# Performance work log

Hardware: AMD Instinct MI355X
Metric: run time of the kernel (lower is better)

The kernel has to match this reference:

```python
import jax, jax.numpy as jnp
import numpy as np

D = 1024
H = 16
HD = D // H  # 64
FF = 4 * D
EPS = 1e-5

def _layernorm(x, g, b):
    mu = jnp.mean(x, axis=-1, keepdims=True)
    var = jnp.mean((x - mu) ** 2, axis=-1, keepdims=True)
    return (x - mu) * jax.lax.rsqrt(var + EPS) * g + b

def _apply_rotary(x, cos, sin):
    # x: [B,H,T,HD]; cos/sin: [T,HD//2] broadcast over B,H
    d = x.shape[-1] // 2
    x1, x2 = x[..., :d], x[..., d:]
    return jnp.concatenate([x1 * cos - x2 * sin, x2 * cos + x1 * sin], axis=-1)

def setup_inputs() -> dict:
    key = jax.random.key(0)
    ks = jax.random.split(key, 12)
    B, T = 4, 2048
    s = 0.02
    return {
        "x": jax.random.normal(ks[0], (B, T, D), jnp.float32),
        "rope_cos": jax.random.uniform(ks[1], (T, HD // 2), jnp.float32),
        "rope_sin": jax.random.uniform(ks[2], (T, HD // 2), jnp.float32),
        "ln1_g": jnp.ones((D,), jnp.float32),
        "ln1_b": jnp.zeros((D,), jnp.float32),
        "Wqkv": jax.random.normal(ks[3], (D, 3 * D), jnp.float32) * s,
        "bqkv": jnp.zeros((3 * D,), jnp.float32),
        "Wo": jax.random.normal(ks[4], (D, D), jnp.float32) * s,
        "bo": jnp.zeros((D,), jnp.float32),
        "ln2_g": jnp.ones((D,), jnp.float32),
        "ln2_b": jnp.zeros((D,), jnp.float32),
        "W1": jax.random.normal(ks[5], (D, FF), jnp.float32) * s,
        "b1": jnp.zeros((FF,), jnp.float32),
        "W2": jax.random.normal(ks[6], (FF, D), jnp.float32) * s,
        "b2": jnp.zeros((D,), jnp.float32),
    }

def reference(x, rope_cos, rope_sin, ln1_g, ln1_b, Wqkv, bqkv, Wo, bo, ln2_g, ln2_b, W1, b1, W2, b2):
    B, T, _ = x.shape
    h = _layernorm(x, ln1_g, ln1_b)
    qkv = (h @ Wqkv + bqkv).reshape(B, T, 3, H, HD)
    qkv = jnp.transpose(qkv, (2, 0, 3, 1, 4))  # [3,B,H,T,HD]
    q, k, v = qkv[0], qkv[1], qkv[2]
    q = _apply_rotary(q, rope_cos, rope_sin)
    k = _apply_rotary(k, rope_cos, rope_sin)
    scale = 1.0 / jnp.sqrt(jnp.float32(HD))
    scores = jnp.einsum('bhqd,bhkd->bhqk', q, k) * scale
    probs = jax.nn.softmax(scores, axis=-1)
    attn = jnp.einsum('bhqk,bhkd->bhqd', probs, v)
    attn = jnp.transpose(attn, (0, 2, 1, 3)).reshape(B, T, D)
    x = x + attn @ Wo + bo
    h2 = _layernorm(x, ln2_g, ln2_b)
    mlp = jax.nn.gelu(h2 @ W1 + b1, approximate=False) @ W2 + b2
    return x + mlp
```

## Files before the change

kernel.cpp:

```cpp
#include <hip/hip_runtime.h>
#include <hip/hip_bf16.h>
#include <math.h>

typedef __bf16 bf16x8 __attribute__((ext_vector_type(8)));
typedef float f32x4 __attribute__((ext_vector_type(4)));
typedef float f32x16 __attribute__((ext_vector_type(16)));
typedef unsigned short u16x8 __attribute__((ext_vector_type(8)));
typedef unsigned short u16x4 __attribute__((ext_vector_type(4)));
typedef unsigned int u32x4 __attribute__((ext_vector_type(4)));

#define DEV __device__ __forceinline__

DEV unsigned short f2bf(float f) { __bf16 h = (__bf16)f; return __builtin_bit_cast(unsigned short, h); }
DEV float bf2f(unsigned short u) { __bf16 h = __builtin_bit_cast(__bf16, u); return (float)h; }
DEV unsigned int pk2(float a, float b) {
  return (unsigned int)f2bf(a) | ((unsigned int)f2bf(b) << 16);
}

DEV void async_cp16(const void* g, void* l) {
  __builtin_amdgcn_global_load_lds((const __attribute__((address_space(1))) void*)g,
                                   (__attribute__((address_space(3))) void*)l, 16, 0, 0);
}


__global__ __launch_bounds__(256) void ln_kernel(const float* __restrict__ in,
    const float* __restrict__ g, const float* __restrict__ b,
    unsigned short* __restrict__ out)
{
  const int row = blockIdx.x;
  const int tid = threadIdx.x;
  const float4 v = ((const float4*)(in + (size_t)row * 1024))[tid];
  float s  = v.x + v.y + v.z + v.w;
  float sq = v.x*v.x + v.y*v.y + v.z*v.z + v.w*v.w;
  for (int m = 1; m < 64; m <<= 1) { s += __shfl_xor(s, m); sq += __shfl_xor(sq, m); }
  __shared__ float red[8];
  const int wave = tid >> 6;
  if ((tid & 63) == 0) { red[wave] = s; red[4 + wave] = sq; }
  __syncthreads();
  s  = red[0] + red[1] + red[2] + red[3];
  sq = red[4] + red[5] + red[6] + red[7];
  const float mu = s * (1.0f / 1024.0f);
  const float var = sq * (1.0f / 1024.0f) - mu * mu;
  const float rs = rsqrtf(var + 1e-5f);
  const float4 gv = ((const float4*)g)[tid];
  const float4 bv = ((const float4*)b)[tid];
  u16x4 o;
  o[0] = f2bf((v.x - mu) * rs * gv.x + bv.x);
  o[1] = f2bf((v.y - mu) * rs * gv.y + bv.y);
  o[2] = f2bf((v.z - mu) * rs * gv.z + bv.z);
  o[3] = f2bf((v.w - mu) * rs * gv.w + bv.w);
  *(u16x4*)(out + (size_t)row * 1024 + tid * 4) = o;
}

__global__ __launch_bounds__(256) void wtrans_kernel(const float* __restrict__ in,
    unsigned short* __restrict__ out, int K, int N)
{
  __shared__ float tile[32][33];
  const int n0 = blockIdx.x * 32, k0 = blockIdx.y * 32;
  const int r = threadIdx.x >> 5, c = threadIdx.x & 31;
  for (int p = 0; p < 4; ++p)
    tile[r + p * 8][c] = in[(size_t)(k0 + r + p * 8) * N + n0 + c];
  __syncthreads();
  for (int p = 0; p < 4; ++p)
    out[(size_t)(n0 + r + p * 8) * K + k0 + c] = f2bf(tile[c][r + p * 8]);
}

enum { EPI_QKV = 0, EPI_ATTNO = 1, EPI_GELU = 2, EPI_FINAL = 3 };

template <int EPI>
__global__ __launch_bounds__(256, 3) void gemm_bt(
    const unsigned short* __restrict__ A,
    const unsigned short* __restrict__ Bt,
    const float* __restrict__ bias,
    const float* __restrict__ resid,
    void* __restrict__ out,
    int M, int N, int K,
    const float* __restrict__ rc, const float* __restrict__ rsn,
    unsigned short* __restrict__ vout)
{
  __shared__ unsigned short lA[8192] __attribute__((aligned(16)));
  __shared__ unsigned short lB[8192] __attribute__((aligned(16)));
  const int tid = threadIdx.x;
  const int lane = tid & 63, wave = tid >> 6;
  const int l15 = lane & 15, quad = lane >> 4;
  const int bm = blockIdx.x * 128, bn = blockIdx.y * 128;
  const int wm = (wave & 1) * 64, wn = (wave >> 1) * 64;

  const unsigned short* ga[4]; const unsigned short* gb[4];
  unsigned short* la_dst[4]; unsigned short* lb_dst[4];
  for (int it = 0; it < 4; ++it) {
    const int s = it * 256 + tid;
    const int row = s >> 3;
    const int ch = (s & 7) ^ (row & 7);
    ga[it] = A  + (size_t)(bm + row) * K + ch * 8;
    gb[it] = Bt + (size_t)(bn + row) * K + ch * 8;
    const int base = (it * 256 + wave * 64) * 8;
    la_dst[it] = lA + base;
    lb_dst[it] = lB + base;
  }
  int offA[2][4], offB[2][4];
  for (int ks = 0; ks < 2; ++ks)
    for (int i = 0; i < 4; ++i) {
      int row = wm + i * 16 + l15;
      offA[ks][i] = (row * 8 + ((ks * 4 + quad) ^ (row & 7))) * 8;
      row = wn + i * 16 + l15;
      offB[ks][i] = (row * 8 + ((ks * 4 + quad) ^ (row & 7))) * 8;
    }

  f32x4 acc[4][4];
  for (int i = 0; i < 4; ++i)
    for (int j = 0; j < 4; ++j)
      acc[i][j] = f32x4{0.f, 0.f, 0.f, 0.f};

  for (int k0 = 0; k0 < K; k0 += 64) {
    for (int it = 0; it < 4; ++it) async_cp16(ga[it], la_dst[it]);
    for (int it = 0; it < 4; ++it) async_cp16(gb[it], lb_dst[it]);
    for (int it = 0; it < 4; ++it) { ga[it] += 64; gb[it] += 64; }
    __syncthreads();
    for (int ks = 0; ks < 2; ++ks) {
      bf16x8 af[4], bfr[4];
      for (int i = 0; i < 4; ++i) af[i]  = *(const bf16x8*)(lA + offA[ks][i]);
      for (int j = 0; j < 4; ++j) bfr[j] = *(const bf16x8*)(lB + offB[ks][j]);
      for (int i = 0; i < 4; ++i)
        for (int j = 0; j < 4; ++j)
          acc[i][j] = __builtin_amdgcn_mfma_f32_16x16x32_bf16(af[i], bfr[j], acc[i][j], 0, 0, 0);
    }
    __syncthreads();
  }

  float bvals[4];
  for (int j = 0; j < 4; ++j) bvals[j] = bias[bn + wn + j * 16 + l15];

  if constexpr (EPI == EPI_QKV) {
    const int cn = bn + wn;
    const int sec = cn >> 10;
    if (sec == 2) {
      const int b = bm >> 11;
      const int hh = (cn & 1023) >> 6;
      for (int i = 0; i < 4; ++i) {
        const int t0 = (bm + wm + i * 16 + quad * 4) & 2047;
        for (int j = 0; j < 4; ++j) {
          const int d = j * 16 + l15;
          u16x4 o;
          for (int r = 0; r < 4; ++r) o[r] = f2bf(acc[i][j][r] + bvals[j]);
          *(u16x4*)(vout + ((size_t)((b * 16 + hh) * 64 + d)) * 2048 + t0) = o;
        }
      }
    } else {
      const float qscale = (sec == 0) ? 0.18033688f : 1.0f;
      unsigned short* qkvout = (unsigned short*)out;
      for (int i = 0; i < 4; ++i) {
        for (int r = 0; r < 4; ++r) {
          const int row = bm + wm + i * 16 + quad * 4 + r;
          const int t = row & 2047;
          for (int j = 0; j < 2; ++j) {
            const int d = j * 16 + l15;
            const float v1 = acc[i][j][r] + bvals[j];
            const float v2 = acc[i][j + 2][r] + bvals[j + 2];
            const float c = rc[t * 32 + d], s = rsn[t * 32 + d];
            const float o1 = (v1 * c - v2 * s) * qscale;
            const float o2 = (v2 * c + v1 * s) * qscale;
            const size_t base = (size_t)row * 3072 + cn + d;
            qkvout[base] = f2bf(o1);
            qkvout[base + 32] = f2bf(o2);
          }
        }
      }
    }
  } else {
    for (int i = 0; i < 4; ++i) {
      for (int r = 0; r < 4; ++r) {
        const size_t row = bm + wm + i * 16 + quad * 4 + r;
        for (int j = 0; j < 4; ++j) {
          const size_t col = bn + wn + j * 16 + l15;
          const float v = acc[i][j][r] + bvals[j];
          const size_t idx = row * (size_t)N + col;
          if constexpr (EPI == EPI_ATTNO) {
            ((float*)out)[idx] = resid[idx] + v;
          } else if constexpr (EPI == EPI_GELU) {
            const float gl = 0.5f * v * (1.0f + erff(v * 0.70710678118f));
            ((unsigned short*)out)[idx] = f2bf(gl);
          } else {
            ((float*)out)[idx] = resid[idx] + v;
          }
        }
      }
    }
  }
}

__global__ __launch_bounds__(256, 4) void attn_kernel(
    const unsigned short* __restrict__ qkv,
    const unsigned short* __restrict__ vt,
    unsigned short* __restrict__ outb)
{
  __shared__ unsigned short Ks[2][4096] __attribute__((aligned(16)));
  __shared__ unsigned short Vs[2][4096] __attribute__((aligned(16)));
  __shared__ float Sred[128];

  const int tid = threadIdx.x;
  const int lane = tid & 63, wave = tid >> 6;
  const int l31 = lane & 31, hl = lane >> 5;
  const int bh = blockIdx.y, b = bh >> 4, h = bh & 15;
  const int q0 = blockIdx.x * 128;
  const int qsub = wave * 32;

  bf16x8 qf[4];
  {
    const unsigned short* qp = qkv + (size_t)(b * 2048 + q0 + qsub + l31) * 3072 + h * 64 + hl * 8;
    for (int kc = 0; kc < 4; ++kc) qf[kc] = *(const bf16x8*)(qp + kc * 16);
  }

  const int s0 = wave * 128 + lane, s1 = s0 + 64;
  const int r0 = s0 >> 3, c0 = (lane & 7) ^ (r0 & 7);
  const int r1 = s1 >> 3, c1 = (lane & 7) ^ (r1 & 7);
  const unsigned short* kbase = qkv + (size_t)(b * 2048) * 3072 + 1024 + h * 64;
  const unsigned short* ks0 = kbase + (size_t)r0 * 3072 + c0 * 8;
  const unsigned short* ks1 = kbase + (size_t)r1 * 3072 + c1 * 8;
  const unsigned short* vbase = vt + (size_t)bh * 64 * 2048;
  const unsigned short* vs0 = vbase + (size_t)r0 * 2048 + c0 * 8;
  const unsigned short* vs1 = vbase + (size_t)r1 * 2048 + c1 * 8;
  unsigned short* kd[2] = { Ks[0] + wave * 1024, Ks[1] + wave * 1024 };
  unsigned short* vd[2] = { Vs[0] + wave * 1024, Vs[1] + wave * 1024 };

  int offK[2][4], offV[2][4];
  for (int g = 0; g < 2; ++g)
    for (int kc = 0; kc < 4; ++kc) {
      const int rk = g * 32 + l31;
      offK[g][kc] = (rk * 8 + ((2 * kc + hl) ^ (rk & 7))) * 8;
    }
  for (int dn = 0; dn < 2; ++dn)
    for (int t = 0; t < 4; ++t) {
      const int rv = dn * 32 + l31;
      offV[dn][t] = (rv * 8 + ((2 * t + hl) ^ (rv & 7))) * 8;
    }

  f32x16 accO[2];
  for (int dn = 0; dn < 2; ++dn)
    for (int i = 0; i < 16; ++i) accO[dn][i] = 0.f;
  float rsum = 0.f;

  async_cp16(ks0, kd[0]);
  async_cp16(ks1, kd[0] + 512);
  async_cp16(vs0, vd[0]);
  async_cp16(vs1, vd[0] + 512);

  for (int kt = 0; kt < 32; ++kt) {
    const int cur = kt & 1, nxt = cur ^ 1;
    __syncthreads();
    if (kt < 31) {
      const size_t ko = (size_t)(kt + 1) * 64 * 3072;
      const int vo = (kt + 1) * 64;
      async_cp16(ks0 + ko, kd[nxt]);
      async_cp16(ks1 + ko, kd[nxt] + 512);
      async_cp16(vs0 + vo, vd[nxt]);
      async_cp16(vs1 + vo, vd[nxt] + 512);
    }
    for (int g = 0; g < 2; ++g) {
      f32x16 accS;
      for (int i = 0; i < 16; ++i) accS[i] = 0.f;
      __builtin_amdgcn_s_setprio(1);
      for (int kc = 0; kc < 4; ++kc) {
        const bf16x8 kf = *(const bf16x8*)(Ks[cur] + offK[g][kc]);
        accS = __builtin_amdgcn_mfma_f32_32x32x16_bf16(kf, qf[kc], accS, 0, 0, 0);
      }
      __builtin_amdgcn_s_setprio(0);
      float p[16];
      for (int i = 0; i < 16; ++i) {
        p[i] = __builtin_amdgcn_exp2f(accS[i]);
        rsum += p[i];
      }
      for (int c = 0; c < 2; ++c) {
        const unsigned int xlo0 = pk2(p[8 * c + 0], p[8 * c + 1]);
        const unsigned int xlo1 = pk2(p[8 * c + 2], p[8 * c + 3]);
        const unsigned int xhi0 = pk2(p[8 * c + 4], p[8 * c + 5]);
        const unsigned int xhi1 = pk2(p[8 * c + 6], p[8 * c + 7]);
        const auto sw0 = __builtin_amdgcn_permlane32_swap(xlo0, xhi0, false, false);
        const auto sw1 = __builtin_amdgcn_permlane32_swap(xlo1, xhi1, false, false);
        u32x4 w;
        w[0] = sw0[0];
        w[1] = sw1[0];
        w[2] = sw0[1];
        w[3] = sw1[1];
        const bf16x8 pf = __builtin_bit_cast(bf16x8, w);
        const int t = 2 * g + c;
        __builtin_amdgcn_s_setprio(1);
        for (int dn = 0; dn < 2; ++dn) {
          const bf16x8 vf = *(const bf16x8*)(Vs[cur] + offV[dn][t]);
          accO[dn] = __builtin_amdgcn_mfma_f32_32x32x16_bf16(pf, vf, accO[dn], 0, 0, 0);
        }
        __builtin_amdgcn_s_setprio(0);
      }
    }
  }

  {
    const float rs2 = rsum + __shfl_xor(rsum, 32);
    if (hl == 0) Sred[qsub + l31] = rs2;
  }
  __syncthreads();
  for (int reg = 0; reg < 16; ++reg) {
    const int rq = qsub + (reg & 3) + 8 * (reg >> 2) + 4 * hl;
    const float inv = 1.0f / Sred[rq];
    const size_t row = (size_t)(b * 2048 + q0 + rq);
    for (int dn = 0; dn < 2; ++dn)
      outb[row * 1024 + h * 64 + dn * 32 + l31] = f2bf(accO[dn][reg] * inv);
  }
}

extern "C" void kernel_launch(void* const* d_in, const int* in_sizes, int n_in,
                              void* d_out, int out_size, void* d_ws, size_t ws_size,
                              hipStream_t stream)
{
  const float* x        = (const float*)d_in[0];
  const float* rope_cos = (const float*)d_in[1];
  const float* rope_sin = (const float*)d_in[2];
  const float* ln1_g    = (const float*)d_in[3];
  const float* ln1_b    = (const float*)d_in[4];
  const float* Wqkv     = (const float*)d_in[5];
  const float* bqkv     = (const float*)d_in[6];
  const float* Wo       = (const float*)d_in[7];
  const float* bo       = (const float*)d_in[8];
  const float* ln2_g    = (const float*)d_in[9];
  const float* ln2_b    = (const float*)d_in[10];
  const float* W1       = (const float*)d_in[11];
  const float* b1       = (const float*)d_in[12];
  const float* W2       = (const float*)d_in[13];
  const float* b2       = (const float*)d_in[14];
  float* outp = (float*)d_out;

  char* ws = (char*)d_ws;
  size_t off = 0;
  auto alloc = [&](size_t bytes) -> void* {
    void* p = ws + off;
    off += (bytes + 255) & ~(size_t)255;
    return p;
  };
  unsigned short* h1    = (unsigned short*)alloc(8192ull * 1024 * 2);
  unsigned short* wqkvT = (unsigned short*)alloc(3072ull * 1024 * 2);
  unsigned short* woT   = (unsigned short*)alloc(1024ull * 1024 * 2);
  unsigned short* w1T   = (unsigned short*)alloc(4096ull * 1024 * 2);
  unsigned short* w2T   = (unsigned short*)alloc(1024ull * 4096 * 2);
  unsigned short* qkv   = (unsigned short*)alloc(8192ull * 3072 * 2);
  unsigned short* vtb   = (unsigned short*)alloc(64ull * 64 * 2048 * 2);
  unsigned short* h2    = (unsigned short*)alloc(8192ull * 1024 * 2);
  unsigned short* ffb   = (unsigned short*)alloc(8192ull * 4096 * 2);

  wtrans_kernel<<<dim3(96, 32), 256, 0, stream>>>(Wqkv, wqkvT, 1024, 3072);
  wtrans_kernel<<<dim3(32, 32), 256, 0, stream>>>(Wo, woT, 1024, 1024);
  wtrans_kernel<<<dim3(128, 32), 256, 0, stream>>>(W1, w1T, 1024, 4096);
  wtrans_kernel<<<dim3(32, 128), 256, 0, stream>>>(W2, w2T, 4096, 1024);

  ln_kernel<<<8192, 256, 0, stream>>>(x, ln1_g, ln1_b, h1);
  gemm_bt<EPI_QKV><<<dim3(64, 24), 256, 0, stream>>>(h1, wqkvT, bqkv, nullptr, qkv,
                                                     8192, 3072, 1024, rope_cos, rope_sin, vtb);
  attn_kernel<<<dim3(16, 64), 256, 0, stream>>>(qkv, vtb, h1);
  gemm_bt<EPI_ATTNO><<<dim3(64, 8), 256, 0, stream>>>(h1, woT, bo, x, d_out,
                                                      8192, 1024, 1024, nullptr, nullptr, nullptr);
  ln_kernel<<<8192, 256, 0, stream>>>(outp, ln2_g, ln2_b, h2);
  gemm_bt<EPI_GELU><<<dim3(64, 32), 256, 0, stream>>>(h2, w1T, b1, nullptr, ffb,
                                                      8192, 4096, 1024, nullptr, nullptr, nullptr);
  gemm_bt<EPI_FINAL><<<dim3(64, 8), 256, 0, stream>>>(ffb, w2T, b2, outp, d_out,
                                                      8192, 1024, 4096, nullptr, nullptr, nullptr);
}
```

Before: 495.8 us.

## Process two 32-row query groups per wave in attention to reuse K/V tiles

Each wave in the attention kernel now handles 64 query rows as two 32-row groups instead of one. Each K fragment and V fragment loaded from LDS feeds two MFMAs. The block covers 256 queries, so the grid is halved and K/V global/LDS traffic per query drops by half. In exchange register pressure roughly doubles (launch bounds lowered to 2 blocks/SM) and there are fewer blocks to fill the GPU (512 blocks).

```diff
diff --git a/kernel.cpp b/kernel.cpp
--- a/kernel.cpp
+++ b/kernel.cpp
@@ -189,26 +189,26 @@
   }
 }
 
-__global__ __launch_bounds__(256, 4) void attn_kernel(
+__global__ __launch_bounds__(256, 2) void attn_kernel(
     const unsigned short* __restrict__ qkv,
     const unsigned short* __restrict__ vt,
     unsigned short* __restrict__ outb)
 {
   __shared__ unsigned short Ks[2][4096] __attribute__((aligned(16)));
   __shared__ unsigned short Vs[2][4096] __attribute__((aligned(16)));
-  __shared__ float Sred[128];
+  __shared__ float Sred[256];
 
   const int tid = threadIdx.x;
   const int lane = tid & 63, wave = tid >> 6;
   const int l31 = lane & 31, hl = lane >> 5;
   const int bh = blockIdx.y, b = bh >> 4, h = bh & 15;
-  const int q0 = blockIdx.x * 128;
-  const int qsub = wave * 32;
-
-  bf16x8 qf[4];
-  {
-    const unsigned short* qp = qkv + (size_t)(b * 2048 + q0 + qsub + l31) * 3072 + h * 64 + hl * 8;
-    for (int kc = 0; kc < 4; ++kc) qf[kc] = *(const bf16x8*)(qp + kc * 16);
+  const int q0 = blockIdx.x * 256;
+  const int qsub = wave * 64;
+
+  bf16x8 qf[2][4];
+  for (int qg = 0; qg < 2; ++qg) {
+    const unsigned short* qp = qkv + (size_t)(b * 2048 + q0 + qsub + qg * 32 + l31) * 3072 + h * 64 + hl * 8;
+    for (int kc = 0; kc < 4; ++kc) qf[qg][kc] = *(const bf16x8*)(qp + kc * 16);
   }
 
   const int s0 = wave * 128 + lane, s1 = s0 + 64;
@@ -235,10 +235,14 @@
       offV[dn][t] = (rv * 8 + ((2 * t + hl) ^ (rv & 7))) * 8;
     }
 
-  f32x16 accO[2];
-  for (int dn = 0; dn < 2; ++dn)
-    for (int i = 0; i < 16; ++i) accO[dn][i] = 0.f;
-  float rsum = 0.f;
+  f32x16 accO[2][2];
+  for (int qg = 0; qg < 2; ++qg)
+    for (int dn = 0; dn < 2; ++dn)
+      for (int i = 0; i < 16; ++i) accO[qg][dn][i] = 0.f;
+  float rsum[2] = {0.f, 0.f};
+
+  f32x16 z16;
+  for (int i = 0; i < 16; ++i) z16[i] = 0.f;
 
   async_cp16(ks0, kd[0]);
   async_cp16(ks1, kd[0] + 512);
@@ -257,55 +261,61 @@
       async_cp16(vs1 + vo, vd[nxt] + 512);
     }
     for (int g = 0; g < 2; ++g) {
-      f32x16 accS;
-      for (int i = 0; i < 16; ++i) accS[i] = 0.f;
-      __builtin_amdgcn_s_setprio(1);
-      for (int kc = 0; kc < 4; ++kc) {
-        const bf16x8 kf = *(const bf16x8*)(Ks[cur] + offK[g][kc]);
-        accS = __builtin_amdgcn_mfma_f32_32x32x16_bf16(kf, qf[kc], accS, 0, 0, 0);
-      }
-      __builtin_amdgcn_s_setprio(0);
-      float p[16];
-      for (int i = 0; i < 16; ++i) {
-        p[i] = __builtin_amdgcn_exp2f(accS[i]);
-        rsum += p[i];
+      bf16x8 kf[4];
+      for (int kc = 0; kc < 4; ++kc) kf[kc] = *(const bf16x8*)(Ks[cur] + offK[g][kc]);
+      bf16x8 pfr[2][2];
+      for (int qg = 0; qg < 2; ++qg) {
+        __builtin_amdgcn_s_setprio(1);
+        f32x16 accS = __builtin_amdgcn_mfma_f32_32x32x16_bf16(kf[0], qf[qg][0], z16, 0, 0, 0);
+        for (int kc = 1; kc < 4; ++kc)
+          accS = __builtin_amdgcn_mfma_f32_32x32x16_bf16(kf[kc], qf[qg][kc], accS, 0, 0, 0);
+        __builtin_amdgcn_s_setprio(0);
+        float p[16];
+        for (int i = 0; i < 16; ++i) {
+          p[i] = __builtin_amdgcn_exp2f(accS[i]);
+          rsum[qg] += p[i];
+        }
+        for (int c = 0; c < 2; ++c) {
+          const unsigned int xlo0 = pk2(p[8 * c + 0], p[8 * c + 1]);
+          const unsigned int xlo1 = pk2(p[8 * c + 2], p[8 * c + 3]);
+          const unsigned int xhi0 = pk2(p[8 * c + 4], p[8 * c + 5]);
+          const unsigned int xhi1 = pk2(p[8 * c + 6], p[8 * c + 7]);
+          const auto sw0 = __builtin_amdgcn_permlane32_swap(xlo0, xhi0, false, false);
+          const auto sw1 = __builtin_amdgcn_permlane32_swap(xlo1, xhi1, false, false);
+          u32x4 w;
+          w[0] = sw0[0];
+          w[1] = sw1[0];
+          w[2] = sw0[1];
+          w[3] = sw1[1];
+          pfr[qg][c] = __builtin_bit_cast(bf16x8, w);
+        }
       }
       for (int c = 0; c < 2; ++c) {
-        const unsigned int xlo0 = pk2(p[8 * c + 0], p[8 * c + 1]);
-        const unsigned int xlo1 = pk2(p[8 * c + 2], p[8 * c + 3]);
-        const unsigned int xhi0 = pk2(p[8 * c + 4], p[8 * c + 5]);
-        const unsigned int xhi1 = pk2(p[8 * c + 6], p[8 * c + 7]);
-        const auto sw0 = __builtin_amdgcn_permlane32_swap(xlo0, xhi0, false, false);
-        const auto sw1 = __builtin_amdgcn_permlane32_swap(xlo1, xhi1, false, false);
-        u32x4 w;
-        w[0] = sw0[0];
-        w[1] = sw1[0];
-        w[2] = sw0[1];
-        w[3] = sw1[1];
-        const bf16x8 pf = __builtin_bit_cast(bf16x8, w);
         const int t = 2 * g + c;
         __builtin_amdgcn_s_setprio(1);
         for (int dn = 0; dn < 2; ++dn) {
           const bf16x8 vf = *(const bf16x8*)(Vs[cur] + offV[dn][t]);
-          accO[dn] = __builtin_amdgcn_mfma_f32_32x32x16_bf16(pf, vf, accO[dn], 0, 0, 0);
+          accO[0][dn] = __builtin_amdgcn_mfma_f32_32x32x16_bf16(pfr[0][c], vf, accO[0][dn], 0, 0, 0);
+          accO[1][dn] = __builtin_amdgcn_mfma_f32_32x32x16_bf16(pfr[1][c], vf, accO[1][dn], 0, 0, 0);
         }
         __builtin_amdgcn_s_setprio(0);
       }
     }
   }
 
-  {
-    const float rs2 = rsum + __shfl_xor(rsum, 32);
-    if (hl == 0) Sred[qsub + l31] = rs2;
+  for (int qg = 0; qg < 2; ++qg) {
+    const float rs2 = rsum[qg] + __shfl_xor(rsum[qg], 32);
+    if (hl == 0) Sred[qsub + qg * 32 + l31] = rs2;
   }
   __syncthreads();
-  for (int reg = 0; reg < 16; ++reg) {
-    const int rq = qsub + (reg & 3) + 8 * (reg >> 2) + 4 * hl;
-    const float inv = 1.0f / Sred[rq];
-    const size_t row = (size_t)(b * 2048 + q0 + rq);
-    for (int dn = 0; dn < 2; ++dn)
-      outb[row * 1024 + h * 64 + dn * 32 + l31] = f2bf(accO[dn][reg] * inv);
-  }
+  for (int qg = 0; qg < 2; ++qg)
+    for (int reg = 0; reg < 16; ++reg) {
+      const int rq = qsub + qg * 32 + (reg & 3) + 8 * (reg >> 2) + 4 * hl;
+      const float inv = 1.0f / Sred[rq];
+      const size_t row = (size_t)(b * 2048 + q0 + rq);
+      for (int dn = 0; dn < 2; ++dn)
+        outb[row * 1024 + h * 64 + dn * 32 + l31] = f2bf(accO[qg][dn][reg] * inv);
+    }
 }
 
 extern "C" void kernel_launch(void* const* d_in, const int* in_sizes, int n_in,
@@ -354,7 +364,7 @@
   ln_kernel<<<8192, 256, 0, stream>>>(x, ln1_g, ln1_b, h1);
   gemm_bt<EPI_QKV><<<dim3(64, 24), 256, 0, stream>>>(h1, wqkvT, bqkv, nullptr, qkv,
                                                      8192, 3072, 1024, rope_cos, rope_sin, vtb);
-  attn_kernel<<<dim3(16, 64), 256, 0, stream>>>(qkv, vtb, h1);
+  attn_kernel<<<dim3(8, 64), 256, 0, stream>>>(qkv, vtb, h1);
   gemm_bt<EPI_ATTNO><<<dim3(64, 8), 256, 0, stream>>>(h1, woT, bo, x, d_out,
                                                       8192, 1024, 1024, nullptr, nullptr, nullptr);
   ln_kernel<<<8192, 256, 0, stream>>>(outp, ln2_g, ln2_b, h2);
```

Measured after the change: 514.3 us. 1.04x slower.
